# Kernel tuning notes

Measured on AMD Instinct MI355X. Metric: run time of the kernel, lower is better.

Reference implementation:

```python
import jax, jax.numpy as jnp
import numpy as np

BATCH, SEQ, D_IN, D_OUT, PALETTE = 4, 2048, 4096, 4096, 256


def setup_inputs() -> dict:
    key = jax.random.key(0)
    k_in, k_w, k_lut, k_b = jax.random.split(key, 4)
    inp = jax.random.normal(k_in, (BATCH, SEQ, D_IN), dtype=jnp.float32)
    # palette indices playing the role of the stored uint8 weight tensor
    weight = jax.random.randint(k_w, (D_OUT, D_IN), 0, PALETTE, dtype=jnp.int32)
    # fp8-derived palette values (simulated as small fp32 centroids)
    lookup_table = jax.random.normal(k_lut, (PALETTE,), dtype=jnp.float32) * 0.02
    bias = jax.random.normal(k_b, (D_OUT,), dtype=jnp.float32) * 0.01
    return {"input": inp, "lookup_table": lookup_table, "weight": weight, "bias": bias}


def reference(input, lookup_table, weight, bias):
    # Dequantize palette indices -> full weight matrix [D_OUT, D_IN]
    full_weights = lookup_table[weight]
    # F.linear: input @ W^T + bias
    out = jnp.einsum("bsd,od->bso", input, full_weights)
    return out + bias
```

## Files before the change

kernel.cpp:

```cpp
#include <hip/hip_runtime.h>
#include <cstdint>


static constexpr int Md = 8192;
static constexpr int Nd = 4096;
static constexpr int Kd = 4096;
static constexpr int NKT = Kd / 64;

typedef _Float16 half8 __attribute__((ext_vector_type(8)));
typedef float f32x4 __attribute__((ext_vector_type(4)));

__device__ __forceinline__ void async_copy16(const _Float16* g, _Float16* l) {
  __builtin_amdgcn_global_load_lds((const __attribute__((address_space(1))) void*)g,
                                   (__attribute__((address_space(3))) void*)l, 16, 0, 0);
}

__device__ __forceinline__ half8 lds_read_b128(uint32_t addr) {
  half8 r;
  asm volatile("ds_read_b128 %0, %1" : "=v"(r) : "v"(addr));
  return r;
}

__global__ __launch_bounds__(256) void cvt_a(const float* __restrict__ in,
                                             _Float16* __restrict__ out) {
  const size_t i = (size_t)blockIdx.x * 256 + threadIdx.x;
  const float4 x = ((const float4*)in)[2 * i];
  const float4 y = ((const float4*)in)[2 * i + 1];
  half8 h;
  h[0] = (_Float16)x.x; h[1] = (_Float16)x.y; h[2] = (_Float16)x.z; h[3] = (_Float16)x.w;
  h[4] = (_Float16)y.x; h[5] = (_Float16)y.y; h[6] = (_Float16)y.z; h[7] = (_Float16)y.w;
  *(half8*)(out + 8 * i) = h;
}

__global__ __launch_bounds__(256) void dequant_b(const int* __restrict__ w,
                                                 const float* __restrict__ lut,
                                                 _Float16* __restrict__ out) {
  __shared__ float slut[256];
  slut[threadIdx.x] = lut[threadIdx.x];
  __syncthreads();
  const size_t i = (size_t)blockIdx.x * 256 + threadIdx.x;
  const int4 a = ((const int4*)w)[2 * i];
  const int4 b = ((const int4*)w)[2 * i + 1];
  half8 h;
  h[0] = (_Float16)slut[a.x]; h[1] = (_Float16)slut[a.y];
  h[2] = (_Float16)slut[a.z]; h[3] = (_Float16)slut[a.w];
  h[4] = (_Float16)slut[b.x]; h[5] = (_Float16)slut[b.y];
  h[6] = (_Float16)slut[b.z]; h[7] = (_Float16)slut[b.w];
  *(half8*)(out + 8 * i) = h;
}

__global__ __launch_bounds__(512, 2) void gemm_f16(const _Float16* __restrict__ A,
                                                   const _Float16* __restrict__ Bt,
                                                   const float* __restrict__ bias,
                                                   float* __restrict__ C) {
  __shared__ __align__(16) _Float16 As[2][256 * 64];
  __shared__ __align__(16) _Float16 Bs[2][256 * 64];

  const int tid = threadIdx.x;
  const int lane = tid & 63;
  const int wave = tid >> 6;
  const int wm = wave >> 2;
  const int wn = wave & 3;

  const int bid0 = blockIdx.x + blockIdx.y * gridDim.x;
  const int bid = (bid0 & 7) * 64 + (bid0 >> 3);
  const int bm = bid & 31;
  const int bn = bid >> 5;

  const int trow = tid >> 3;
  const int tcol = tid & 7;
  const int gch = tcol ^ (trow & 7);
  const _Float16* ag = A + (size_t)(bm * 256 + trow) * Kd + gch * 8;
  const _Float16* bg = Bt + (size_t)(bn * 256 + trow) * Kd + gch * 8;
  const int lds_off = trow * 64 + tcol * 8;

  auto stage = [&](int buf, int kt) {
#pragma unroll
    for (int ht = 0; ht < 4; ++ht) {
      async_copy16(ag + (size_t)kt * 64 + (size_t)ht * (64 * Kd),
                   &As[buf][lds_off + ht * 4096]);
      async_copy16(bg + (size_t)kt * 64 + (size_t)ht * (64 * Kd),
                   &Bs[buf][lds_off + ht * 4096]);
    }
  };

  const int fr = lane & 15;
  const int fq = lane >> 4;
  const int e = fr & 7;
  const uint32_t as0 = (uint32_t)(uintptr_t)&As[0][0];
  const uint32_t bs0 = (uint32_t)(uintptr_t)&Bs[0][0];
  const uint32_t s0b = (uint32_t)((fq ^ e) * 16);
  const uint32_t s1b = (uint32_t)(((4 | fq) ^ e) * 16);
  const uint32_t arow = as0 + (uint32_t)((wm * 128 + fr) * 128);
  const uint32_t brow = bs0 + (uint32_t)((wn * 64 + fr) * 128);

  f32x4 acc[8][4] = {};

  stage(0, 0);

  for (int kt = 0; kt < NKT; ++kt) {
    const uint32_t cb = (uint32_t)(kt & 1) * 32768u;
    if (kt + 1 < NKT) {
      stage((kt & 1) ^ 1, kt + 1);
      asm volatile("s_waitcnt vmcnt(8)" ::: "memory");
    } else {
      asm volatile("s_waitcnt vmcnt(0)" ::: "memory");
    }
    __builtin_amdgcn_s_barrier();

    const uint32_t a0 = arow + cb + s0b;
    const uint32_t a1 = arow + cb + s1b;
    const uint32_t b0a = brow + cb + s0b;
    const uint32_t b1a = brow + cb + s1b;

    half8 a[4][2], b0[2][2], b1[2][2];

#pragma unroll
    for (int i = 0; i < 4; ++i) {
      a[i][0] = lds_read_b128(a0 + i * 2048);
      a[i][1] = lds_read_b128(a1 + i * 2048);
    }
#pragma unroll
    for (int j = 0; j < 2; ++j) {
      b0[j][0] = lds_read_b128(b0a + j * 2048);
      b0[j][1] = lds_read_b128(b1a + j * 2048);
    }
    __builtin_amdgcn_s_barrier();
    asm volatile("s_waitcnt lgkmcnt(0)" ::: "memory");
    __builtin_amdgcn_sched_barrier(0);
    __builtin_amdgcn_s_setprio(1);
#pragma unroll
    for (int i = 0; i < 4; ++i)
#pragma unroll
      for (int j = 0; j < 2; ++j) {
        acc[i][j] = __builtin_amdgcn_mfma_f32_16x16x32_f16(a[i][0], b0[j][0], acc[i][j], 0, 0, 0);
        acc[i][j] = __builtin_amdgcn_mfma_f32_16x16x32_f16(a[i][1], b0[j][1], acc[i][j], 0, 0, 0);
      }
    __builtin_amdgcn_s_setprio(0);
    __builtin_amdgcn_s_barrier();

#pragma unroll
    for (int j = 0; j < 2; ++j) {
      b1[j][0] = lds_read_b128(b0a + 4096 + j * 2048);
      b1[j][1] = lds_read_b128(b1a + 4096 + j * 2048);
    }
    __builtin_amdgcn_s_barrier();
    asm volatile("s_waitcnt lgkmcnt(0)" ::: "memory");
    __builtin_amdgcn_sched_barrier(0);
    __builtin_amdgcn_s_setprio(1);
#pragma unroll
    for (int i = 0; i < 4; ++i)
#pragma unroll
      for (int j = 0; j < 2; ++j) {
        acc[i][2 + j] = __builtin_amdgcn_mfma_f32_16x16x32_f16(a[i][0], b1[j][0], acc[i][2 + j], 0, 0, 0);
        acc[i][2 + j] = __builtin_amdgcn_mfma_f32_16x16x32_f16(a[i][1], b1[j][1], acc[i][2 + j], 0, 0, 0);
      }
    __builtin_amdgcn_s_setprio(0);
    __builtin_amdgcn_s_barrier();

#pragma unroll
    for (int i = 0; i < 4; ++i) {
      a[i][0] = lds_read_b128(a0 + 8192 + i * 2048);
      a[i][1] = lds_read_b128(a1 + 8192 + i * 2048);
    }
    __builtin_amdgcn_s_barrier();
    asm volatile("s_waitcnt lgkmcnt(0)" ::: "memory");
    __builtin_amdgcn_sched_barrier(0);
    __builtin_amdgcn_s_setprio(1);
#pragma unroll
    for (int i = 0; i < 4; ++i)
#pragma unroll
      for (int j = 0; j < 2; ++j) {
        acc[4 + i][2 + j] = __builtin_amdgcn_mfma_f32_16x16x32_f16(a[i][0], b1[j][0], acc[4 + i][2 + j], 0, 0, 0);
        acc[4 + i][2 + j] = __builtin_amdgcn_mfma_f32_16x16x32_f16(a[i][1], b1[j][1], acc[4 + i][2 + j], 0, 0, 0);
      }
    __builtin_amdgcn_s_setprio(0);
    __builtin_amdgcn_s_barrier();

    __builtin_amdgcn_s_setprio(1);
#pragma unroll
    for (int i = 0; i < 4; ++i)
#pragma unroll
      for (int j = 0; j < 2; ++j) {
        acc[4 + i][j] = __builtin_amdgcn_mfma_f32_16x16x32_f16(a[i][0], b0[j][0], acc[4 + i][j], 0, 0, 0);
        acc[4 + i][j] = __builtin_amdgcn_mfma_f32_16x16x32_f16(a[i][1], b0[j][1], acc[4 + i][j], 0, 0, 0);
      }
    __builtin_amdgcn_s_setprio(0);
    __builtin_amdgcn_s_barrier();
  }

  const int ccol0 = bn * 256 + wn * 64 + fr;
  const int crow0 = bm * 256 + wm * 128 + fq * 4;
  float bv[4];
#pragma unroll
  for (int j = 0; j < 4; ++j) bv[j] = bias[ccol0 + j * 16];
#pragma unroll
  for (int i = 0; i < 8; ++i) {
#pragma unroll
    for (int r = 0; r < 4; ++r) {
      float* cp = C + (size_t)(crow0 + i * 16 + r) * Nd + ccol0;
#pragma unroll
      for (int j = 0; j < 4; ++j) cp[j * 16] = acc[i][j][r] + bv[j];
    }
  }
}

extern "C" void kernel_launch(void* const* d_in, const int* in_sizes, int n_in,
                              void* d_out, int out_size, void* d_ws, size_t ws_size,
                              hipStream_t stream) {
  const float* inp = (const float*)d_in[0];
  const float* lut = (const float*)d_in[1];
  const int* wgt = (const int*)d_in[2];
  const float* bias = (const float*)d_in[3];
  float* out = (float*)d_out;

  _Float16* Ah = (_Float16*)d_ws;
  _Float16* Bh = (_Float16*)d_ws + (size_t)Md * Kd;

  cvt_a<<<(Md * (size_t)Kd) / (8 * 256), 256, 0, stream>>>(inp, Ah);
  dequant_b<<<((size_t)Nd * Kd) / (8 * 256), 256, 0, stream>>>(wgt, lut, Bh);

  dim3 grid(Md / 256, Nd / 256);
  gemm_f16<<<grid, 512, 0, stream>>>(Ah, Bh, bias, out);
}
```

Before: 530.6 us.

## Switch GEMM to 32x32x16 MFMA with double-buffered register fragments

The 16x16x32 MFMA tiles are replaced with 32x32x16 tiles, which lowers the number of LDS reads per FLOP. The main loop is restructured so LDS fragment reads for the next k-slice (register sets A/B) overlap the MFMAs on the current slice, with partial lgkmcnt waits instead of full drains. Global prefetch is now issued at k-tile pairs within the unrolled loop. The cost is a more complex barrier schedule and higher register pressure, with some risk that the waits or LDS buffer reuse are subtly wrong.

```diff
diff --git a/kernel.cpp b/kernel.cpp
--- a/kernel.cpp
+++ b/kernel.cpp
@@ -8,7 +8,7 @@
 static constexpr int NKT = Kd / 64;
 
 typedef _Float16 half8 __attribute__((ext_vector_type(8)));
-typedef float f32x4 __attribute__((ext_vector_type(4)));
+typedef float f32x16 __attribute__((ext_vector_type(16)));
 
 __device__ __forceinline__ void async_copy16(const _Float16* g, _Float16* l) {
   __builtin_amdgcn_global_load_lds((const __attribute__((address_space(1))) void*)g,
@@ -20,6 +20,11 @@
   asm volatile("ds_read_b128 %0, %1" : "=v"(r) : "v"(addr));
   return r;
 }
+
+#define LGKM(n) asm volatile("s_waitcnt lgkmcnt(" #n ")" ::: "memory")
+#define VMCNT(n) asm volatile("s_waitcnt vmcnt(" #n ")" ::: "memory")
+#define BAR() __builtin_amdgcn_s_barrier()
+#define SB0() __builtin_amdgcn_sched_barrier(0)
 
 __global__ __launch_bounds__(256) void cvt_a(const float* __restrict__ in,
                                              _Float16* __restrict__ out) {
@@ -84,123 +89,110 @@
     }
   };
 
-  const int fr = lane & 15;
-  const int fq = lane >> 4;
-  const int e = fr & 7;
+  const int l31 = lane & 31;
+  const int hi = lane >> 5;
+  const int e = lane & 7;
   const uint32_t as0 = (uint32_t)(uintptr_t)&As[0][0];
   const uint32_t bs0 = (uint32_t)(uintptr_t)&Bs[0][0];
-  const uint32_t s0b = (uint32_t)((fq ^ e) * 16);
-  const uint32_t s1b = (uint32_t)(((4 | fq) ^ e) * 16);
-  const uint32_t arow = as0 + (uint32_t)((wm * 128 + fr) * 128);
-  const uint32_t brow = bs0 + (uint32_t)((wn * 64 + fr) * 128);
-
-  f32x4 acc[8][4] = {};
+  uint32_t ab[2][4], bb[2][4];
+#pragma unroll
+  for (int s = 0; s < 4; ++s) {
+    const uint32_t off = (uint32_t)((((2 * s) + hi) ^ e) * 16);
+    ab[0][s] = as0 + (uint32_t)((wm * 128 + l31) * 128) + off;
+    ab[1][s] = ab[0][s] + 32768u;
+    bb[0][s] = bs0 + (uint32_t)((wn * 64 + l31) * 128) + off;
+    bb[1][s] = bb[0][s] + 32768u;
+  }
+
+  half8 aA[4], bA[2], aB[4], bB[2];
+  f32x16 acc[4][2] = {};
+
+#define READS(SET, AB, BB)                  \
+  a##SET[0] = lds_read_b128((AB));          \
+  a##SET[1] = lds_read_b128((AB) + 4096);   \
+  a##SET[2] = lds_read_b128((AB) + 8192);   \
+  a##SET[3] = lds_read_b128((AB) + 12288);  \
+  b##SET[0] = lds_read_b128((BB));          \
+  b##SET[1] = lds_read_b128((BB) + 4096);
+
+#define MFMAS(SET)                                                                            \
+  acc[0][0] = __builtin_amdgcn_mfma_f32_32x32x16_f16(a##SET[0], b##SET[0], acc[0][0], 0, 0, 0); \
+  acc[0][1] = __builtin_amdgcn_mfma_f32_32x32x16_f16(a##SET[0], b##SET[1], acc[0][1], 0, 0, 0); \
+  acc[1][0] = __builtin_amdgcn_mfma_f32_32x32x16_f16(a##SET[1], b##SET[0], acc[1][0], 0, 0, 0); \
+  acc[1][1] = __builtin_amdgcn_mfma_f32_32x32x16_f16(a##SET[1], b##SET[1], acc[1][1], 0, 0, 0); \
+  acc[2][0] = __builtin_amdgcn_mfma_f32_32x32x16_f16(a##SET[2], b##SET[0], acc[2][0], 0, 0, 0); \
+  acc[2][1] = __builtin_amdgcn_mfma_f32_32x32x16_f16(a##SET[2], b##SET[1], acc[2][1], 0, 0, 0); \
+  acc[3][0] = __builtin_amdgcn_mfma_f32_32x32x16_f16(a##SET[3], b##SET[0], acc[3][0], 0, 0, 0); \
+  acc[3][1] = __builtin_amdgcn_mfma_f32_32x32x16_f16(a##SET[3], b##SET[1], acc[3][1], 0, 0, 0);
+
+#define PHASE(RSET, AB, BB, CSET)       \
+  READS(RSET, AB, BB);                  \
+  BAR();                                \
+  LGKM(6);                              \
+  SB0();                                \
+  __builtin_amdgcn_s_setprio(1);        \
+  MFMAS(CSET);                          \
+  __builtin_amdgcn_s_setprio(0);        \
+  BAR();
 
   stage(0, 0);
-
-  for (int kt = 0; kt < NKT; ++kt) {
-    const uint32_t cb = (uint32_t)(kt & 1) * 32768u;
-    if (kt + 1 < NKT) {
-      stage((kt & 1) ^ 1, kt + 1);
-      asm volatile("s_waitcnt vmcnt(8)" ::: "memory");
+  stage(1, 1);
+  VMCNT(8);
+  BAR();
+  READS(A, ab[0][0], bb[0][0]);
+
+  for (int kt = 0; kt < NKT; kt += 2) {
+    PHASE(B, ab[0][1], bb[0][1], A);
+    PHASE(A, ab[0][2], bb[0][2], B);
+    PHASE(B, ab[0][3], bb[0][3], A);
+    VMCNT(0);
+    BAR();
+    READS(A, ab[1][0], bb[1][0]);
+    if (kt + 2 < NKT) stage(0, kt + 2);
+    BAR();
+    LGKM(6);
+    SB0();
+    __builtin_amdgcn_s_setprio(1);
+    MFMAS(B);
+    __builtin_amdgcn_s_setprio(0);
+    BAR();
+
+    PHASE(B, ab[1][1], bb[1][1], A);
+    PHASE(A, ab[1][2], bb[1][2], B);
+    PHASE(B, ab[1][3], bb[1][3], A);
+    if (kt + 2 < NKT) {
+      VMCNT(0);
+      BAR();
+      READS(A, ab[0][0], bb[0][0]);
+      if (kt + 3 < NKT) stage(1, kt + 3);
+      BAR();
+      LGKM(6);
+      SB0();
+      __builtin_amdgcn_s_setprio(1);
+      MFMAS(B);
+      __builtin_amdgcn_s_setprio(0);
+      BAR();
     } else {
-      asm volatile("s_waitcnt vmcnt(0)" ::: "memory");
+      LGKM(0);
+      SB0();
+      __builtin_amdgcn_s_setprio(1);
+      MFMAS(B);
+      __builtin_amdgcn_s_setprio(0);
     }
-    __builtin_amdgcn_s_barrier();
-
-    const uint32_t a0 = arow + cb + s0b;
-    const uint32_t a1 = arow + cb + s1b;
-    const uint32_t b0a = brow + cb + s0b;
-    const uint32_t b1a = brow + cb + s1b;
-
-    half8 a[4][2], b0[2][2], b1[2][2];
-
-#pragma unroll
-    for (int i = 0; i < 4; ++i) {
-      a[i][0] = lds_read_b128(a0 + i * 2048);
-      a[i][1] = lds_read_b128(a1 + i * 2048);
-    }
-#pragma unroll
-    for (int j = 0; j < 2; ++j) {
-      b0[j][0] = lds_read_b128(b0a + j * 2048);
-      b0[j][1] = lds_read_b128(b1a + j * 2048);
-    }
-    __builtin_amdgcn_s_barrier();
-    asm volatile("s_waitcnt lgkmcnt(0)" ::: "memory");
-    __builtin_amdgcn_sched_barrier(0);
-    __builtin_amdgcn_s_setprio(1);
-#pragma unroll
-    for (int i = 0; i < 4; ++i)
-#pragma unroll
-      for (int j = 0; j < 2; ++j) {
-        acc[i][j] = __builtin_amdgcn_mfma_f32_16x16x32_f16(a[i][0], b0[j][0], acc[i][j], 0, 0, 0);
-        acc[i][j] = __builtin_amdgcn_mfma_f32_16x16x32_f16(a[i][1], b0[j][1], acc[i][j], 0, 0, 0);
-      }
-    __builtin_amdgcn_s_setprio(0);
-    __builtin_amdgcn_s_barrier();
-
-#pragma unroll
-    for (int j = 0; j < 2; ++j) {
-      b1[j][0] = lds_read_b128(b0a + 4096 + j * 2048);
-      b1[j][1] = lds_read_b128(b1a + 4096 + j * 2048);
-    }
-    __builtin_amdgcn_s_barrier();
-    asm volatile("s_waitcnt lgkmcnt(0)" ::: "memory");
-    __builtin_amdgcn_sched_barrier(0);
-    __builtin_amdgcn_s_setprio(1);
-#pragma unroll
-    for (int i = 0; i < 4; ++i)
-#pragma unroll
-      for (int j = 0; j < 2; ++j) {
-        acc[i][2 + j] = __builtin_amdgcn_mfma_f32_16x16x32_f16(a[i][0], b1[j][0], acc[i][2 + j], 0, 0, 0);
-        acc[i][2 + j] = __builtin_amdgcn_mfma_f32_16x16x32_f16(a[i][1], b1[j][1], acc[i][2 + j], 0, 0, 0);
-      }
-    __builtin_amdgcn_s_setprio(0);
-    __builtin_amdgcn_s_barrier();
-
-#pragma unroll
-    for (int i = 0; i < 4; ++i) {
-      a[i][0] = lds_read_b128(a0 + 8192 + i * 2048);
-      a[i][1] = lds_read_b128(a1 + 8192 + i * 2048);
-    }
-    __builtin_amdgcn_s_barrier();
-    asm volatile("s_waitcnt lgkmcnt(0)" ::: "memory");
-    __builtin_amdgcn_sched_barrier(0);
-    __builtin_amdgcn_s_setprio(1);
-#pragma unroll
-    for (int i = 0; i < 4; ++i)
-#pragma unroll
-      for (int j = 0; j < 2; ++j) {
-        acc[4 + i][2 + j] = __builtin_amdgcn_mfma_f32_16x16x32_f16(a[i][0], b1[j][0], acc[4 + i][2 + j], 0, 0, 0);
-        acc[4 + i][2 + j] = __builtin_amdgcn_mfma_f32_16x16x32_f16(a[i][1], b1[j][1], acc[4 + i][2 + j], 0, 0, 0);
-      }
-    __builtin_amdgcn_s_setprio(0);
-    __builtin_amdgcn_s_barrier();
-
-    __builtin_amdgcn_s_setprio(1);
-#pragma unroll
-    for (int i = 0; i < 4; ++i)
-#pragma unroll
-      for (int j = 0; j < 2; ++j) {
-        acc[4 + i][j] = __builtin_amdgcn_mfma_f32_16x16x32_f16(a[i][0], b0[j][0], acc[4 + i][j], 0, 0, 0);
-        acc[4 + i][j] = __builtin_amdgcn_mfma_f32_16x16x32_f16(a[i][1], b0[j][1], acc[4 + i][j], 0, 0, 0);
-      }
-    __builtin_amdgcn_s_setprio(0);
-    __builtin_amdgcn_s_barrier();
   }
 
-  const int ccol0 = bn * 256 + wn * 64 + fr;
-  const int crow0 = bm * 256 + wm * 128 + fq * 4;
-  float bv[4];
-#pragma unroll
-  for (int j = 0; j < 4; ++j) bv[j] = bias[ccol0 + j * 16];
-#pragma unroll
-  for (int i = 0; i < 8; ++i) {
-#pragma unroll
-    for (int r = 0; r < 4; ++r) {
-      float* cp = C + (size_t)(crow0 + i * 16 + r) * Nd + ccol0;
-#pragma unroll
-      for (int j = 0; j < 4; ++j) cp[j * 16] = acc[i][j][r] + bv[j];
+  const int ccol0 = bn * 256 + wn * 64 + l31;
+  const int crow0 = bm * 256 + wm * 128 + hi * 4;
+  const float bv0 = bias[ccol0];
+  const float bv1 = bias[ccol0 + 32];
+#pragma unroll
+  for (int m = 0; m < 4; ++m) {
+#pragma unroll
+    for (int r = 0; r < 16; ++r) {
+      const int row = crow0 + m * 32 + (r & 3) + 8 * (r >> 2);
+      float* cp = C + (size_t)row * Nd + ccol0;
+      cp[0] = acc[m][0][r] + bv0;
+      cp[32] = acc[m][1][r] + bv1;
     }
   }
 }
```

New measurement: 735.9 us. 38.7% more time.
